# Performance work log

Hardware: AMD Instinct MI355X
Metric: run time of the kernel (lower is better)

The kernel has to match this reference:

```python
import jax, jax.numpy as jnp
import numpy as np

NUM_NODES = 116
EMBED = 64
HIDDEN = 64
OUT_FEAT = 116


def mish(x):
    return x * jnp.tanh(jax.nn.softplus(x))


def sage_conv(x, src, dst, w_l, b_l, w_r, n):
    # PyG SAGEConv (mean aggr): out = lin_l(mean_{j->i} x_j) + lin_r(x_i)
    agg = jax.ops.segment_sum(x[src], dst, num_segments=n)
    cnt = jax.ops.segment_sum(jnp.ones((src.shape[0],), x.dtype), dst, num_segments=n)
    mean = agg / jnp.clip(cnt, 1.0)[:, None]
    return mean @ w_l.T + b_l + x @ w_r.T


def setup_inputs() -> dict:
    key = jax.random.key(0)
    ks = jax.random.split(key, 12)
    B = 64
    N = B * NUM_NODES          # 7424 total nodes
    E = N * 32                 # 237568 edges
    d_in = EMBED * NUM_NODES   # 7424
    d_hid = HIDDEN * NUM_NODES # 7424
    d_out = OUT_FEAT * NUM_NODES  # 13456

    def lin_w(k, fan_out, fan_in):
        s = 1.0 / np.sqrt(fan_in)
        return jax.random.uniform(k, (fan_out, fan_in), jnp.float32, -s, s)

    return {
        "z": jax.random.normal(ks[0], (N, EMBED), jnp.float32),
        "edge_index": jax.random.randint(ks[1], (2, E), 0, N, jnp.int64),
        "batch_size": B,
        "w1_l": lin_w(ks[2], EMBED, EMBED),
        "b1_l": jnp.zeros((EMBED,), jnp.float32),
        "w1_r": lin_w(ks[3], EMBED, EMBED),
        "w2_l": lin_w(ks[4], EMBED, EMBED),
        "b2_l": jnp.zeros((EMBED,), jnp.float32),
        "w2_r": lin_w(ks[5], EMBED, EMBED),
        "fc1_w": lin_w(ks[6], d_hid, d_in),
        "fc1_b": jax.random.uniform(ks[7], (d_hid,), jnp.float32, -1/np.sqrt(d_in), 1/np.sqrt(d_in)),
        "fc2_w": lin_w(ks[8], d_out, d_hid),
        "fc2_b": jax.random.uniform(ks[9], (d_out,), jnp.float32, -1/np.sqrt(d_hid), 1/np.sqrt(d_hid)),
    }


def reference(z, edge_index, batch_size, w1_l, b1_l, w1_r, w2_l, b2_l, w2_r,
              fc1_w, fc1_b, fc2_w, fc2_b):
    n = z.shape[0]
    src, dst = edge_index[0], edge_index[1]
    h = mish(sage_conv(z, src, dst, w1_l, b1_l, w1_r, n))
    h = mish(sage_conv(h, src, dst, w2_l, b2_l, w2_r, n))
    h_flat = h.reshape(batch_size, NUM_NODES * EMBED)
    hidden = mish(h_flat @ fc1_w.T + fc1_b)
    x_rec = (hidden @ fc2_w.T + fc2_b).reshape(batch_size, NUM_NODES, OUT_FEAT)
    # enforce symmetry, unit diagonal
    sym = 0.5 * (x_rec + jnp.swapaxes(x_rec, 1, 2))
    eye = jnp.eye(NUM_NODES, dtype=bool)[None]
    sym = jnp.where(eye, jnp.asarray(1.0, sym.dtype), sym)
    return sym.reshape(batch_size * NUM_NODES, OUT_FEAT)
```

## Files before the change

### kernel.cpp

```cpp
#include <hip/hip_runtime.h>
#include <math.h>

#define NODES_TOT 7424
#define EDGES     237568
#define BATCH     64
#define NN        116
#define KDIM      7424
#define N1        7424
#define N2        13456
#define NKB       116
#define KSPLIT1   16
#define KSPLIT2   8

typedef __attribute__((ext_vector_type(8))) short bf16x8;
typedef __attribute__((ext_vector_type(4))) float f32x4;
typedef __attribute__((ext_vector_type(4))) short s16x4;

__device__ __forceinline__ float mish_f(float v) {
    float sp = fmaxf(v, 0.0f) + log1pf(expf(-fabsf(v)));
    return v * tanhf(sp);
}

__device__ __forceinline__ unsigned short bf_rne(float f) {
    unsigned u = __float_as_uint(f);
    u += 0x7fffu + ((u >> 16) & 1u);
    return (unsigned short)(u >> 16);
}

__global__ void zero_kernel(int* __restrict__ p, int n) {
    int i = blockIdx.x * 256 + threadIdx.x;
    if (i < n) p[i] = 0;
}

__global__ void hist_kernel(const int* __restrict__ dst, int* __restrict__ hist) {
    int e = blockIdx.x * 256 + threadIdx.x;
    if (e < EDGES) atomicAdd(&hist[dst[e]], 1);
}

__global__ void scan_kernel(const int* __restrict__ hist, int* __restrict__ row_start,
                            int* __restrict__ cursor) {
    __shared__ int s[1024];
    int t = threadIdx.x;
    int base = t * 8;
    int loc[8];
    int sum = 0;
    #pragma unroll
    for (int c = 0; c < 8; ++c) {
        int idx = base + c;
        int v = (idx < NODES_TOT) ? hist[idx] : 0;
        loc[c] = sum;
        sum += v;
    }
    s[t] = sum;
    __syncthreads();
    for (int off = 1; off < 1024; off <<= 1) {
        int v = (t >= off) ? s[t - off] : 0;
        __syncthreads();
        s[t] += v;
        __syncthreads();
    }
    int excl = s[t] - sum;
    #pragma unroll
    for (int c = 0; c < 8; ++c) {
        int idx = base + c;
        if (idx < NODES_TOT) {
            int r = excl + loc[c];
            row_start[idx] = r;
            cursor[idx] = r;
        }
    }
}

__global__ void csr_fill_kernel(const int* __restrict__ src, const int* __restrict__ dst,
                                int* __restrict__ cursor, int* __restrict__ csr_src) {
    int e = blockIdx.x * 256 + threadIdx.x;
    if (e < EDGES) {
        int p = atomicAdd(&cursor[dst[e]], 1);
        csr_src[p] = src[e];
    }
}

template <bool BF>
__global__ void __launch_bounds__(256) conv_kernel(
        const float* __restrict__ x, const int* __restrict__ csr_src,
        const int* __restrict__ row_start, const int* __restrict__ deg_arr,
        const float* __restrict__ w_l, const float* __restrict__ b_l,
        const float* __restrict__ w_r, void* __restrict__ h_out_v) {
    __shared__ float wlT[64 * 64];
    __shared__ float wrT[64 * 64];
    __shared__ float mv[4][64];
    __shared__ float xv[4][64];
    int t = threadIdx.x;
    for (int i = 0; i < 16; ++i) {
        int idx = t + i * 256;
        int f = idx >> 6, k = idx & 63;
        wlT[k * 64 + f] = w_l[idx];
        wrT[k * 64 + f] = w_r[idx];
    }
    int g = t >> 6, f = t & 63;
    __syncthreads();
    for (int nb = blockIdx.x * 4; nb < NODES_TOT; nb += gridDim.x * 4) {
        int node = nb + g;
        int deg = deg_arr[node];
        int rs = row_start[node];
        float sum = 0.f;
        for (int e = 0; e < deg; ++e) {
            int s = csr_src[rs + e];
            sum += x[s * 64 + f];
        }
        float mean = sum / (float)max(deg, 1);
        mv[g][f] = mean;
        xv[g][f] = x[node * 64 + f];
        __syncthreads();
        float o = b_l[f];
        #pragma unroll
        for (int k = 0; k < 64; ++k) {
            o = fmaf(mv[g][k], wlT[k * 64 + f], o);
            o = fmaf(xv[g][k], wrT[k * 64 + f], o);
        }
        float m = mish_f(o);
        if (BF) ((unsigned short*)h_out_v)[node * 64 + f] = bf_rne(m);
        else    ((float*)h_out_v)[node * 64 + f] = m;
        __syncthreads();
    }
}

template <int KSHIFT>
__global__ void __launch_bounds__(256) gemm_tile(
        const unsigned short* __restrict__ Abf, const float* __restrict__ W,
        float* __restrict__ Cp, int N) {
    __shared__ __align__(16) short Wsh[512 * 8];
    int t = threadIdx.x;
    int bx = blockIdx.x, by = blockIdx.y;
    int kb0 = (by * NKB) >> KSHIFT;
    int kb1 = ((by + 1) * NKB) >> KSHIFT;
    int n0 = bx * 64;
    int r = t >> 2, q = t & 3;
    int wr = n0 + r; if (wr >= N) wr = N - 1;
    const float* wsrc = W + (size_t)wr * KDIM + q * 4;
    int half = q & 1;
    int fbase = q >> 1;
    int wv = t >> 6, l = t & 63, l15 = l & 15, hi = l >> 4;
    f32x4 acc[4];
    #pragma unroll
    for (int g = 0; g < 4; ++g) acc[g] = (f32x4){0.f, 0.f, 0.f, 0.f};

    f32x4 w[4];
    {
        size_t k0 = (size_t)kb0 * 64;
        #pragma unroll
        for (int i = 0; i < 4; ++i) w[i] = *(const f32x4*)(wsrc + k0 + i * 16);
    }
    for (int kb = kb0; kb < kb1; ++kb) {
        s16x4 cv[4];
        #pragma unroll
        for (int i = 0; i < 4; ++i)
            #pragma unroll
            for (int j = 0; j < 4; ++j) cv[i][j] = (short)bf_rne(w[i][j]);
        __syncthreads();
        #pragma unroll
        for (int i = 0; i < 4; ++i)
            *(s16x4*)&Wsh[((i * 2 + fbase) * 64 + r) * 8 + half * 4] = cv[i];
        __syncthreads();
        if (kb + 1 < kb1) {
            size_t kn = (size_t)(kb + 1) * 64;
            #pragma unroll
            for (int i = 0; i < 4; ++i) w[i] = *(const f32x4*)(wsrc + kn + i * 16);
        }
        size_t k0 = (size_t)kb * 64;
        #pragma unroll
        for (int s = 0; s < 2; ++s) {
            int fw = s * 4 + hi;
            bf16x8 bh = *(const bf16x8*)&Wsh[(fw * 64 + wv * 16 + l15) * 8];
            #pragma unroll
            for (int g = 0; g < 4; ++g) {
                bf16x8 av = *(const bf16x8*)(Abf + (size_t)(g * 16 + l15) * KDIM + k0 + fw * 8);
                acc[g] = __builtin_amdgcn_mfma_f32_16x16x32_bf16(av, bh, acc[g], 0, 0, 0);
            }
        }
    }
    int gn = n0 + wv * 16 + l15;
    if (gn < N) {
        float* cp = Cp + (size_t)by * 64 * N;
        #pragma unroll
        for (int g = 0; g < 4; ++g)
            #pragma unroll
            for (int rr = 0; rr < 4; ++rr)
                cp[(size_t)(g * 16 + hi * 4 + rr) * N + gn] = acc[g][rr];
    }
}

__global__ void reduce1_kernel(const float* __restrict__ Cp, const float* __restrict__ b,
                               unsigned short* __restrict__ A2) {
    int i4 = (blockIdx.x * 256 + threadIdx.x) * 4;
    if (i4 >= BATCH * N1) return;
    int n = i4 % N1;
    f32x4 acc = *(const f32x4*)(b + n);
    #pragma unroll
    for (int s = 0; s < KSPLIT1; ++s)
        acc += *(const f32x4*)(Cp + (size_t)s * BATCH * N1 + i4);
    s16x4 o;
    #pragma unroll
    for (int j = 0; j < 4; ++j) o[j] = (short)bf_rne(mish_f(acc[j]));
    *(s16x4*)(A2 + i4) = o;
}

__global__ void reduce2_kernel(const float* __restrict__ Cp, const float* __restrict__ b,
                               float* __restrict__ C2) {
    int i4 = (blockIdx.x * 256 + threadIdx.x) * 4;
    if (i4 >= BATCH * N2) return;
    int n = i4 % N2;
    f32x4 acc = *(const f32x4*)(b + n);
    #pragma unroll
    for (int s = 0; s < KSPLIT2; ++s)
        acc += *(const f32x4*)(Cp + (size_t)s * BATCH * N2 + i4);
    *(f32x4*)(C2 + i4) = acc;
}

__global__ void sym_kernel(const float* __restrict__ C2, float* __restrict__ out) {
    int tid = blockIdx.x * 256 + threadIdx.x;
    if (tid >= BATCH * NN * NN) return;
    int j = tid % NN;
    int r = tid / NN;
    int i = r % NN;
    int b = r / NN;
    float v;
    if (i == j) {
        v = 1.0f;
    } else {
        v = 0.5f * (C2[(size_t)b * N2 + i * NN + j] + C2[(size_t)b * N2 + j * NN + i]);
    }
    out[tid] = v;
}

extern "C" void kernel_launch(void* const* d_in, const int* in_sizes, int n_in,
                              void* d_out, int out_size, void* d_ws, size_t ws_size,
                              hipStream_t stream) {
    const float* z     = (const float*)d_in[0];
    const int*   edge  = (const int*)d_in[1];
    const float* w1_l  = (const float*)d_in[3];
    const float* b1_l  = (const float*)d_in[4];
    const float* w1_r  = (const float*)d_in[5];
    const float* w2_l  = (const float*)d_in[6];
    const float* b2_l  = (const float*)d_in[7];
    const float* w2_r  = (const float*)d_in[8];
    const float* fc1_w = (const float*)d_in[9];
    const float* fc1_b = (const float*)d_in[10];
    const float* fc2_w = (const float*)d_in[11];
    const float* fc2_b = (const float*)d_in[12];
    float* out = (float*)d_out;

    char* ws = (char*)d_ws;
    size_t off = 0;
    auto alloc = [&](size_t bytes) {
        void* p = ws + off;
        off = (off + bytes + 255) & ~(size_t)255;
        return p;
    };
    int*            hist      = (int*)alloc(NODES_TOT * 4);
    int*            row_start = (int*)alloc(NODES_TOT * 4);
    int*            cursor    = (int*)alloc(NODES_TOT * 4);
    int*            csr_src   = (int*)alloc((size_t)EDGES * 4);
    float*          h1        = (float*)alloc((size_t)NODES_TOT * 64 * 4);
    unsigned short* A1        = (unsigned short*)alloc((size_t)NODES_TOT * 64 * 2);
    float*          Cp1       = (float*)alloc((size_t)KSPLIT1 * BATCH * N1 * 4);
    unsigned short* A2        = (unsigned short*)alloc((size_t)BATCH * N1 * 2);
    float*          Cp2       = (float*)alloc((size_t)KSPLIT2 * BATCH * N2 * 4);
    float*          C2        = (float*)alloc((size_t)BATCH * N2 * 4);

    const int* src = edge;
    const int* dst = edge + EDGES;

    zero_kernel<<<(NODES_TOT + 255) / 256, 256, 0, stream>>>(hist, NODES_TOT);
    hist_kernel<<<(EDGES + 255) / 256, 256, 0, stream>>>(dst, hist);
    scan_kernel<<<1, 1024, 0, stream>>>(hist, row_start, cursor);
    csr_fill_kernel<<<(EDGES + 255) / 256, 256, 0, stream>>>(src, dst, cursor, csr_src);

    conv_kernel<false><<<928, 256, 0, stream>>>(z, csr_src, row_start, hist, w1_l, b1_l, w1_r, h1);
    conv_kernel<true><<<928, 256, 0, stream>>>(h1, csr_src, row_start, hist, w2_l, b2_l, w2_r, A1);

    gemm_tile<4><<<dim3(N1 / 64, KSPLIT1), 256, 0, stream>>>(A1, fc1_w, Cp1, N1);
    reduce1_kernel<<<(BATCH * N1 / 4 + 255) / 256, 256, 0, stream>>>(Cp1, fc1_b, A2);

    gemm_tile<3><<<dim3((N2 + 63) / 64, KSPLIT2), 256, 0, stream>>>(A2, fc2_w, Cp2, N2);
    reduce2_kernel<<<(BATCH * N2 / 4 + 255) / 256, 256, 0, stream>>>(Cp2, fc2_b, C2);

    sym_kernel<<<(BATCH * NN * NN + 255) / 256, 256, 0, stream>>>(C2, out);
}
```

Measured before the change: 390.4 us.

## Double-buffer weight and activation tiles in LDS and reduce fc1 split-K

The fc GEMM kernel now stages both the fp32->bf16 converted weight tile and the bf16 activation tile in double-buffered LDS. Global loads for the next two K-steps are issued ahead of the MFMA phase, and the barrier is a custom lgkmcnt wait plus s_barrier. Activation reads previously went straight to global memory; they now come from shared memory. fc1's split-K drops from 16 to 8, which halves the partial-sum traffic and reduce work but gives the first GEMM fewer blocks to spread across the chip.

After: 324.4 us. 1.2x faster.

```diff
diff --git a/kernel.cpp b/kernel.cpp
--- a/kernel.cpp
+++ b/kernel.cpp
@@ -9,8 +9,7 @@
 #define N1        7424
 #define N2        13456
 #define NKB       116
-#define KSPLIT1   16
-#define KSPLIT2   8
+#define KSPLIT    8
 
 typedef __attribute__((ext_vector_type(8))) short bf16x8;
 typedef __attribute__((ext_vector_type(4))) float f32x4;
@@ -129,56 +128,99 @@
 __global__ void __launch_bounds__(256) gemm_tile(
         const unsigned short* __restrict__ Abf, const float* __restrict__ W,
         float* __restrict__ Cp, int N) {
-    __shared__ __align__(16) short Wsh[512 * 8];
+    __shared__ __align__(16) short Wsh[2][4096];
+    __shared__ __align__(16) short Ash[2][4096];
     int t = threadIdx.x;
     int bx = blockIdx.x, by = blockIdx.y;
     int kb0 = (by * NKB) >> KSHIFT;
     int kb1 = ((by + 1) * NKB) >> KSHIFT;
+    int S = kb1 - kb0;
     int n0 = bx * 64;
     int r = t >> 2, q = t & 3;
     int wr = n0 + r; if (wr >= N) wr = N - 1;
-    const float* wsrc = W + (size_t)wr * KDIM + q * 4;
-    int half = q & 1;
-    int fbase = q >> 1;
+    const float*          wsrc = W   + (size_t)wr * KDIM + (size_t)kb0 * 64 + q * 4;
+    const unsigned short* asrc = Abf + (size_t)r  * KDIM + (size_t)kb0 * 64 + q * 8;
+    int fb = q >> 1, hf = q & 1;
     int wv = t >> 6, l = t & 63, l15 = l & 15, hi = l >> 4;
     f32x4 acc[4];
     #pragma unroll
     for (int g = 0; g < 4; ++g) acc[g] = (f32x4){0.f, 0.f, 0.f, 0.f};
 
-    f32x4 w[4];
-    {
-        size_t k0 = (size_t)kb0 * 64;
-        #pragma unroll
-        for (int i = 0; i < 4; ++i) w[i] = *(const f32x4*)(wsrc + k0 + i * 16);
-    }
-    for (int kb = kb0; kb < kb1; ++kb) {
-        s16x4 cv[4];
-        #pragma unroll
-        for (int i = 0; i < 4; ++i)
-            #pragma unroll
-            for (int j = 0; j < 4; ++j) cv[i][j] = (short)bf_rne(w[i][j]);
-        __syncthreads();
-        #pragma unroll
-        for (int i = 0; i < 4; ++i)
-            *(s16x4*)&Wsh[((i * 2 + fbase) * 64 + r) * 8 + half * 4] = cv[i];
-        __syncthreads();
-        if (kb + 1 < kb1) {
-            size_t kn = (size_t)(kb + 1) * 64;
-            #pragma unroll
-            for (int i = 0; i < 4; ++i) w[i] = *(const f32x4*)(wsrc + kn + i * 16);
-        }
-        size_t k0 = (size_t)kb * 64;
-        #pragma unroll
-        for (int s = 0; s < 2; ++s) {
-            int fw = s * 4 + hi;
-            bf16x8 bh = *(const bf16x8*)&Wsh[(fw * 64 + wv * 16 + l15) * 8];
-            #pragma unroll
-            for (int g = 0; g < 4; ++g) {
-                bf16x8 av = *(const bf16x8*)(Abf + (size_t)(g * 16 + l15) * KDIM + k0 + fw * 8);
-                acc[g] = __builtin_amdgcn_mfma_f32_16x16x32_bf16(av, bh, acc[g], 0, 0, 0);
-            }
-        }
-    }
+    f32x4 wA0, wA1, wA2, wA3, wB0, wB1, wB2, wB3;
+    bf16x8 aA0, aA1, aB0, aB1;
+
+#define ISSUE(W0, W1, W2, W3, A0, A1, step) do {                          \
+        size_t kk = (size_t)(step) * 64;                                  \
+        W0 = *(const f32x4*)(wsrc + kk);                                  \
+        W1 = *(const f32x4*)(wsrc + kk + 16);                             \
+        W2 = *(const f32x4*)(wsrc + kk + 32);                             \
+        W3 = *(const f32x4*)(wsrc + kk + 48);                             \
+        A0 = *(const bf16x8*)(asrc + kk);                                 \
+        A1 = *(const bf16x8*)(asrc + kk + 32);                            \
+    } while (0)
+
+#define CONVWRITE(W0, W1, W2, W3, A0, A1, b) do {                         \
+        s16x4 cv0, cv1, cv2, cv3;                                         \
+        _Pragma("unroll")                                                 \
+        for (int j = 0; j < 4; ++j) {                                     \
+            cv0[j] = (short)bf_rne(W0[j]);                                \
+            cv1[j] = (short)bf_rne(W1[j]);                                \
+            cv2[j] = (short)bf_rne(W2[j]);                                \
+            cv3[j] = (short)bf_rne(W3[j]);                                \
+        }                                                                 \
+        *(s16x4*)&Wsh[b][((0 * 2 + fb) * 64 + r) * 8 + hf * 4] = cv0;     \
+        *(s16x4*)&Wsh[b][((1 * 2 + fb) * 64 + r) * 8 + hf * 4] = cv1;     \
+        *(s16x4*)&Wsh[b][((2 * 2 + fb) * 64 + r) * 8 + hf * 4] = cv2;     \
+        *(s16x4*)&Wsh[b][((3 * 2 + fb) * 64 + r) * 8 + hf * 4] = cv3;     \
+        *(bf16x8*)&Ash[b][(q * 64 + r) * 8] = A0;                         \
+        *(bf16x8*)&Ash[b][((q + 4) * 64 + r) * 8] = A1;                   \
+    } while (0)
+
+#define MFMAPH(b) do {                                                    \
+        _Pragma("unroll")                                                 \
+        for (int s = 0; s < 2; ++s) {                                     \
+            int fw = s * 4 + hi;                                          \
+            bf16x8 bh = *(const bf16x8*)&Wsh[b][(fw * 64 + wv * 16 + l15) * 8]; \
+            _Pragma("unroll")                                             \
+            for (int g = 0; g < 4; ++g) {                                 \
+                bf16x8 av = *(const bf16x8*)&Ash[b][(fw * 64 + g * 16 + l15) * 8]; \
+                acc[g] = __builtin_amdgcn_mfma_f32_16x16x32_bf16(av, bh, acc[g], 0, 0, 0); \
+            }                                                             \
+        }                                                                 \
+    } while (0)
+
+#define BAR() asm volatile("s_waitcnt lgkmcnt(0)\n\ts_barrier" ::: "memory")
+
+    ISSUE(wA0, wA1, wA2, wA3, aA0, aA1, 0);
+    ISSUE(wB0, wB1, wB2, wB3, aB0, aB1, 1);
+    CONVWRITE(wA0, wA1, wA2, wA3, aA0, aA1, 0);
+    BAR();
+
+    int i = 0;
+    for (; i + 1 < S - 1; i += 2) {
+        if (i + 2 < S) ISSUE(wA0, wA1, wA2, wA3, aA0, aA1, i + 2);
+        MFMAPH(0);
+        CONVWRITE(wB0, wB1, wB2, wB3, aB0, aB1, 1);
+        BAR();
+        if (i + 3 < S) ISSUE(wB0, wB1, wB2, wB3, aB0, aB1, i + 3);
+        MFMAPH(1);
+        CONVWRITE(wA0, wA1, wA2, wA3, aA0, aA1, 0);
+        BAR();
+    }
+    if (i < S - 1) {
+        MFMAPH(0);
+        CONVWRITE(wB0, wB1, wB2, wB3, aB0, aB1, 1);
+        BAR();
+        MFMAPH(1);
+    } else {
+        MFMAPH(0);
+    }
+
+#undef ISSUE
+#undef CONVWRITE
+#undef MFMAPH
+#undef BAR
+
     int gn = n0 + wv * 16 + l15;
     if (gn < N) {
         float* cp = Cp + (size_t)by * 64 * N;
@@ -197,7 +239,7 @@
     int n = i4 % N1;
     f32x4 acc = *(const f32x4*)(b + n);
     #pragma unroll
-    for (int s = 0; s < KSPLIT1; ++s)
+    for (int s = 0; s < KSPLIT; ++s)
         acc += *(const f32x4*)(Cp + (size_t)s * BATCH * N1 + i4);
     s16x4 o;
     #pragma unroll
@@ -212,7 +254,7 @@
     int n = i4 % N2;
     f32x4 acc = *(const f32x4*)(b + n);
     #pragma unroll
-    for (int s = 0; s < KSPLIT2; ++s)
+    for (int s = 0; s < KSPLIT; ++s)
         acc += *(const f32x4*)(Cp + (size_t)s * BATCH * N2 + i4);
     *(f32x4*)(C2 + i4) = acc;
 }
@@ -263,9 +305,9 @@
     int*            csr_src   = (int*)alloc((size_t)EDGES * 4);
     float*          h1        = (float*)alloc((size_t)NODES_TOT * 64 * 4);
     unsigned short* A1        = (unsigned short*)alloc((size_t)NODES_TOT * 64 * 2);
-    float*          Cp1       = (float*)alloc((size_t)KSPLIT1 * BATCH * N1 * 4);
+    float*          Cp1       = (float*)alloc((size_t)KSPLIT * BATCH * N1 * 4);
     unsigned short* A2        = (unsigned short*)alloc((size_t)BATCH * N1 * 2);
-    float*          Cp2       = (float*)alloc((size_t)KSPLIT2 * BATCH * N2 * 4);
+    float*          Cp2       = (float*)alloc((size_t)KSPLIT * BATCH * N2 * 4);
     float*          C2        = (float*)alloc((size_t)BATCH * N2 * 4);
 
     const int* src = edge;
@@ -279,10 +321,10 @@
     conv_kernel<false><<<928, 256, 0, stream>>>(z, csr_src, row_start, hist, w1_l, b1_l, w1_r, h1);
     conv_kernel<true><<<928, 256, 0, stream>>>(h1, csr_src, row_start, hist, w2_l, b2_l, w2_r, A1);
 
-    gemm_tile<4><<<dim3(N1 / 64, KSPLIT1), 256, 0, stream>>>(A1, fc1_w, Cp1, N1);
+    gemm_tile<3><<<dim3(N1 / 64, KSPLIT), 256, 0, stream>>>(A1, fc1_w, Cp1, N1);
     reduce1_kernel<<<(BATCH * N1 / 4 + 255) / 256, 256, 0, stream>>>(Cp1, fc1_b, A2);
 
-    gemm_tile<3><<<dim3((N2 + 63) / 64, KSPLIT2), 256, 0, stream>>>(A2, fc2_w, Cp2, N2);
+    gemm_tile<3><<<dim3((N2 + 63) / 64, KSPLIT), 256, 0, stream>>>(A2, fc2_w, Cp2, N2);
     reduce2_kernel<<<(BATCH * N2 / 4 + 255) / 256, 256, 0, stream>>>(Cp2, fc2_b, C2);
 
     sym_kernel<<<(BATCH * NN * NN + 255) / 256, 256, 0, stream>>>(C2, out);
```

## Stream GEMM operand tiles via global_load_lds double buffering and halve K-split

Applied to the files above, without the earlier changes.

Replaces the register-staged weight tile loader with direct global-to-LDS DMA loads (global_load_lds) for both the fp32 weight tile and the bf16 activation tile. The loads are double-buffered, with XOR swizzles to avoid bank conflicts and a vmcnt-based wait scheme. Weights are now converted to bf16 after being read from LDS instead of before the LDS store. The K-split factors are halved, which gives fewer partial-sum buffers to reduce but also fewer blocks to fill the device.

Measured after the change: 333.5 us. -14.6%, faster.

```diff
diff --git a/kernel.cpp b/kernel.cpp
--- a/kernel.cpp
+++ b/kernel.cpp
@@ -9,8 +9,8 @@
 #define N1        7424
 #define N2        13456
 #define NKB       116
-#define KSPLIT1   16
-#define KSPLIT2   8
+#define KSPLIT1   8
+#define KSPLIT2   4
 
 typedef __attribute__((ext_vector_type(8))) short bf16x8;
 typedef __attribute__((ext_vector_type(4))) float f32x4;
@@ -25,6 +25,12 @@
     unsigned u = __float_as_uint(f);
     u += 0x7fffu + ((u >> 16) & 1u);
     return (unsigned short)(u >> 16);
+}
+
+__device__ __forceinline__ void gload_lds16(const void* g, void* l) {
+    __builtin_amdgcn_global_load_lds(
+        (const __attribute__((address_space(1))) void*)g,
+        (__attribute__((address_space(3))) void*)l, 16, 0, 0);
 }
 
 __global__ void zero_kernel(int* __restrict__ p, int n) {
@@ -125,60 +131,104 @@
     }
 }
 
-template <int KSHIFT>
-__global__ void __launch_bounds__(256) gemm_tile(
+template <int KS>
+__global__ void __launch_bounds__(256) gemm_dma(
         const unsigned short* __restrict__ Abf, const float* __restrict__ W,
         float* __restrict__ Cp, int N) {
-    __shared__ __align__(16) short Wsh[512 * 8];
+    __shared__ __align__(16) float          Wlds[2][4096];
+    __shared__ __align__(16) unsigned short Alds[2][4096];
     int t = threadIdx.x;
     int bx = blockIdx.x, by = blockIdx.y;
-    int kb0 = (by * NKB) >> KSHIFT;
-    int kb1 = ((by + 1) * NKB) >> KSHIFT;
+    int kb0 = (by * NKB) / KS;
+    int kb1 = ((by + 1) * NKB) / KS;
+    int S = kb1 - kb0;
     int n0 = bx * 64;
-    int r = t >> 2, q = t & 3;
-    int wr = n0 + r; if (wr >= N) wr = N - 1;
-    const float* wsrc = W + (size_t)wr * KDIM + q * 4;
-    int half = q & 1;
-    int fbase = q >> 1;
     int wv = t >> 6, l = t & 63, l15 = l & 15, hi = l >> 4;
+
+    const float* wsrc[4];
+    #pragma unroll
+    for (int ii = 0; ii < 4; ++ii) {
+        int rloc = wv * 16 + ii * 4 + (l >> 4);
+        int wr = n0 + rloc; if (wr >= N) wr = N - 1;
+        int g = (l & 15) ^ ((rloc & 7) << 1);
+        wsrc[ii] = W + (size_t)wr * KDIM + (size_t)kb0 * 64 + g * 4;
+    }
+    const unsigned short* asrcp[2];
+    #pragma unroll
+    for (int ii = 0; ii < 2; ++ii) {
+        int rloc = wv * 16 + ii * 8 + (l >> 3);
+        int g = (l & 7) ^ (rloc & 7);
+        asrcp[ii] = Abf + (size_t)rloc * KDIM + (size_t)kb0 * 64 + g * 8;
+    }
+
     f32x4 acc[4];
     #pragma unroll
     for (int g = 0; g < 4; ++g) acc[g] = (f32x4){0.f, 0.f, 0.f, 0.f};
 
-    f32x4 w[4];
-    {
-        size_t k0 = (size_t)kb0 * 64;
-        #pragma unroll
-        for (int i = 0; i < 4; ++i) w[i] = *(const f32x4*)(wsrc + k0 + i * 16);
-    }
-    for (int kb = kb0; kb < kb1; ++kb) {
-        s16x4 cv[4];
-        #pragma unroll
-        for (int i = 0; i < 4; ++i)
-            #pragma unroll
-            for (int j = 0; j < 4; ++j) cv[i][j] = (short)bf_rne(w[i][j]);
-        __syncthreads();
-        #pragma unroll
-        for (int i = 0; i < 4; ++i)
-            *(s16x4*)&Wsh[((i * 2 + fbase) * 64 + r) * 8 + half * 4] = cv[i];
-        __syncthreads();
-        if (kb + 1 < kb1) {
-            size_t kn = (size_t)(kb + 1) * 64;
-            #pragma unroll
-            for (int i = 0; i < 4; ++i) w[i] = *(const f32x4*)(wsrc + kn + i * 16);
-        }
-        size_t k0 = (size_t)kb * 64;
-        #pragma unroll
-        for (int s = 0; s < 2; ++s) {
-            int fw = s * 4 + hi;
-            bf16x8 bh = *(const bf16x8*)&Wsh[(fw * 64 + wv * 16 + l15) * 8];
-            #pragma unroll
-            for (int g = 0; g < 4; ++g) {
-                bf16x8 av = *(const bf16x8*)(Abf + (size_t)(g * 16 + l15) * KDIM + k0 + fw * 8);
-                acc[g] = __builtin_amdgcn_mfma_f32_16x16x32_bf16(av, bh, acc[g], 0, 0, 0);
-            }
-        }
-    }
+#define ISSUE(step, buf) do {                                              \
+        size_t ko = (size_t)(step) * 64;                                   \
+        _Pragma("unroll")                                                  \
+        for (int ii = 0; ii < 4; ++ii)                                     \
+            gload_lds16(wsrc[ii] + ko, &Wlds[buf][(wv * 16 + ii * 4) * 64]); \
+        _Pragma("unroll")                                                  \
+        for (int ii = 0; ii < 2; ++ii)                                     \
+            gload_lds16(asrcp[ii] + ko, &Alds[buf][(wv * 16 + ii * 8) * 64]); \
+    } while (0)
+
+#define MFMAPH(buf) do {                                                   \
+        _Pragma("unroll")                                                  \
+        for (int s = 0; s < 2; ++s) {                                      \
+            int fw = s * 4 + hi;                                           \
+            int n = wv * 16 + l15;                                         \
+            int g0 = (2 * fw) ^ ((n & 7) << 1);                            \
+            f32x4 wlo = *(const f32x4*)&Wlds[buf][n * 64 + g0 * 4];        \
+            f32x4 whi = *(const f32x4*)&Wlds[buf][n * 64 + g0 * 4 + 4];    \
+            bf16x8 bh;                                                     \
+            _Pragma("unroll")                                              \
+            for (int j = 0; j < 4; ++j) {                                  \
+                bh[j]     = (short)bf_rne(wlo[j]);                         \
+                bh[4 + j] = (short)bf_rne(whi[j]);                         \
+            }                                                              \
+            _Pragma("unroll")                                              \
+            for (int g = 0; g < 4; ++g) {                                  \
+                int ar = g * 16 + l15;                                     \
+                bf16x8 av = *(const bf16x8*)&Alds[buf][ar * 64 + ((fw ^ (ar & 7)) * 8)]; \
+                acc[g] = __builtin_amdgcn_mfma_f32_16x16x32_bf16(av, bh, acc[g], 0, 0, 0); \
+            }                                                              \
+        }                                                                  \
+    } while (0)
+
+#define WAIT6()  asm volatile("s_waitcnt vmcnt(6)" ::: "memory")
+#define WAIT0()  asm volatile("s_waitcnt vmcnt(0)" ::: "memory")
+#define RBAR()   asm volatile("s_barrier" ::: "memory")
+#define LBAR()   asm volatile("s_waitcnt lgkmcnt(0)\n\ts_barrier" ::: "memory")
+
+    ISSUE(0, 0);
+    ISSUE(1, 1);
+    WAIT6();
+    RBAR();
+
+    int i = 0;
+    while (true) {
+        MFMAPH(0);
+        LBAR();
+        if (i + 2 < S) { ISSUE(i + 2, 0); WAIT6(); } else { WAIT0(); }
+        RBAR();
+        if (++i == S) break;
+        MFMAPH(1);
+        LBAR();
+        if (i + 2 < S) { ISSUE(i + 2, 1); WAIT6(); } else { WAIT0(); }
+        RBAR();
+        if (++i == S) break;
+    }
+
+#undef ISSUE
+#undef MFMAPH
+#undef WAIT6
+#undef WAIT0
+#undef RBAR
+#undef LBAR
+
     int gn = n0 + wv * 16 + l15;
     if (gn < N) {
         float* cp = Cp + (size_t)by * 64 * N;
@@ -279,10 +329,10 @@
     conv_kernel<false><<<928, 256, 0, stream>>>(z, csr_src, row_start, hist, w1_l, b1_l, w1_r, h1);
     conv_kernel<true><<<928, 256, 0, stream>>>(h1, csr_src, row_start, hist, w2_l, b2_l, w2_r, A1);
 
-    gemm_tile<4><<<dim3(N1 / 64, KSPLIT1), 256, 0, stream>>>(A1, fc1_w, Cp1, N1);
+    gemm_dma<KSPLIT1><<<dim3(N1 / 64, KSPLIT1), 256, 0, stream>>>(A1, fc1_w, Cp1, N1);
     reduce1_kernel<<<(BATCH * N1 / 4 + 255) / 256, 256, 0, stream>>>(Cp1, fc1_b, A2);
 
-    gemm_tile<3><<<dim3((N2 + 63) / 64, KSPLIT2), 256, 0, stream>>>(A2, fc2_w, Cp2, N2);
+    gemm_dma<KSPLIT2><<<dim3((N2 + 63) / 64, KSPLIT2), 256, 0, stream>>>(A2, fc2_w, Cp2, N2);
     reduce2_kernel<<<(BATCH * N2 / 4 + 255) / 256, 256, 0, stream>>>(Cp2, fc2_b, C2);
 
     sym_kernel<<<(BATCH * NN * NN + 255) / 256, 256, 0, stream>>>(C2, out);
```

## Double-buffer larger K chunks in weight GEMM with fewer split-K partitions

Applied to the files above, without the earlier changes.

Replaces the per-64-element K step GEMM with a kernel that stages 256-wide K super-blocks of the fp32 weights, converted to bf16, into a double-buffered LDS array. The next chunk's global loads overlap the current chunk's MFMAs, and activation loads are software-pipelined. Split-K factors drop from 16/8 to 4/2, which shrinks the partial-sum buffers the reduce kernels must read. The cost is fewer blocks in the grid (less parallelism to hide latency), higher register pressure from 16 f32x4 prefetch registers, and a hand-written waitcnt/barrier.

Result: slower. 423.5 us (+8.5%).

```diff
diff --git a/kernel.cpp b/kernel.cpp
--- a/kernel.cpp
+++ b/kernel.cpp
@@ -8,9 +8,9 @@
 #define KDIM      7424
 #define N1        7424
 #define N2        13456
-#define NKB       116
-#define KSPLIT1   16
-#define KSPLIT2   8
+#define SUPER     29
+#define KSPLIT1   4
+#define KSPLIT2   2
 
 typedef __attribute__((ext_vector_type(8))) short bf16x8;
 typedef __attribute__((ext_vector_type(4))) float f32x4;
@@ -125,60 +125,93 @@
     }
 }
 
-template <int KSHIFT>
-__global__ void __launch_bounds__(256) gemm_tile(
+template <int KS>
+__global__ void __launch_bounds__(256, 2) gemm_big(
         const unsigned short* __restrict__ Abf, const float* __restrict__ W,
         float* __restrict__ Cp, int N) {
-    __shared__ __align__(16) short Wsh[512 * 8];
+    __shared__ __align__(16) unsigned short Wlds[2][16384];
     int t = threadIdx.x;
     int bx = blockIdx.x, by = blockIdx.y;
-    int kb0 = (by * NKB) >> KSHIFT;
-    int kb1 = ((by + 1) * NKB) >> KSHIFT;
+    int sb0 = (by * SUPER) / KS;
+    int sb1 = ((by + 1) * SUPER) / KS;
+    int S = sb1 - sb0;
     int n0 = bx * 64;
     int r = t >> 2, q = t & 3;
     int wr = n0 + r; if (wr >= N) wr = N - 1;
-    const float* wsrc = W + (size_t)wr * KDIM + q * 4;
-    int half = q & 1;
-    int fbase = q >> 1;
+    const float* wsrc = W + (size_t)wr * KDIM + (size_t)sb0 * 256 + q * 4;
     int wv = t >> 6, l = t & 63, l15 = l & 15, hi = l >> 4;
+    const unsigned short* arow[4];
+    #pragma unroll
+    for (int g = 0; g < 4; ++g)
+        arow[g] = Abf + (size_t)(g * 16 + l15) * KDIM + (size_t)sb0 * 256 + hi * 8;
+
     f32x4 acc[4];
     #pragma unroll
     for (int g = 0; g < 4; ++g) acc[g] = (f32x4){0.f, 0.f, 0.f, 0.f};
 
-    f32x4 w[4];
-    {
-        size_t k0 = (size_t)kb0 * 64;
-        #pragma unroll
-        for (int i = 0; i < 4; ++i) w[i] = *(const f32x4*)(wsrc + k0 + i * 16);
-    }
-    for (int kb = kb0; kb < kb1; ++kb) {
-        s16x4 cv[4];
-        #pragma unroll
-        for (int i = 0; i < 4; ++i)
-            #pragma unroll
-            for (int j = 0; j < 4; ++j) cv[i][j] = (short)bf_rne(w[i][j]);
-        __syncthreads();
-        #pragma unroll
-        for (int i = 0; i < 4; ++i)
-            *(s16x4*)&Wsh[((i * 2 + fbase) * 64 + r) * 8 + half * 4] = cv[i];
-        __syncthreads();
-        if (kb + 1 < kb1) {
-            size_t kn = (size_t)(kb + 1) * 64;
-            #pragma unroll
-            for (int i = 0; i < 4; ++i) w[i] = *(const f32x4*)(wsrc + kn + i * 16);
+    f32x4 w[16];
+
+#define LOADW(s) do {                                                      \
+        size_t ko = (size_t)(s) * 256;                                     \
+        _Pragma("unroll")                                                  \
+        for (int j = 0; j < 16; ++j)                                       \
+            w[j] = *(const f32x4*)(wsrc + ko + j * 16);                    \
+    } while (0)
+
+#define CONVW(nb) do {                                                     \
+        _Pragma("unroll")                                                  \
+        for (int j = 0; j < 16; ++j) {                                     \
+            s16x4 cv;                                                      \
+            _Pragma("unroll")                                              \
+            for (int e = 0; e < 4; ++e) cv[e] = (short)bf_rne(w[j][e]);    \
+            *(s16x4*)&Wlds[nb][((2 * j + (q >> 1)) * 64 + r) * 8 + (q & 1) * 4] = cv; \
+        }                                                                  \
+    } while (0)
+
+#define MFMA_STEP(b, s) do {                                               \
+        size_t ko = (size_t)(s) * 256;                                     \
+        bf16x8 a0 = *(const bf16x8*)(arow[0] + ko);                        \
+        bf16x8 a1 = *(const bf16x8*)(arow[1] + ko);                        \
+        bf16x8 a2 = *(const bf16x8*)(arow[2] + ko);                        \
+        bf16x8 a3 = *(const bf16x8*)(arow[3] + ko);                        \
+        _Pragma("unroll")                                                  \
+        for (int kk = 0; kk < 8; ++kk) {                                   \
+            bf16x8 n0_, n1_, n2_, n3_;                                     \
+            if (kk < 7) {                                                  \
+                n0_ = *(const bf16x8*)(arow[0] + ko + (kk + 1) * 32);      \
+                n1_ = *(const bf16x8*)(arow[1] + ko + (kk + 1) * 32);      \
+                n2_ = *(const bf16x8*)(arow[2] + ko + (kk + 1) * 32);      \
+                n3_ = *(const bf16x8*)(arow[3] + ko + (kk + 1) * 32);      \
+            }                                                              \
+            bf16x8 bh = *(const bf16x8*)&Wlds[b][((kk * 4 + hi) * 64 + wv * 16 + l15) * 8]; \
+            acc[0] = __builtin_amdgcn_mfma_f32_16x16x32_bf16(a0, bh, acc[0], 0, 0, 0); \
+            acc[1] = __builtin_amdgcn_mfma_f32_16x16x32_bf16(a1, bh, acc[1], 0, 0, 0); \
+            acc[2] = __builtin_amdgcn_mfma_f32_16x16x32_bf16(a2, bh, acc[2], 0, 0, 0); \
+            acc[3] = __builtin_amdgcn_mfma_f32_16x16x32_bf16(a3, bh, acc[3], 0, 0, 0); \
+            if (kk < 7) { a0 = n0_; a1 = n1_; a2 = n2_; a3 = n3_; }        \
+        }                                                                  \
+    } while (0)
+
+#define LBAR() asm volatile("s_waitcnt lgkmcnt(0)\n\ts_barrier" ::: "memory")
+
+    LOADW(0);
+    CONVW(0);
+    LBAR();
+    for (int s = 0; s < S; ++s) {
+        int b = s & 1;
+        if (s + 1 < S) LOADW(s + 1);
+        MFMA_STEP(b, s);
+        if (s + 1 < S) {
+            CONVW(b ^ 1);
+            LBAR();
         }
-        size_t k0 = (size_t)kb * 64;
-        #pragma unroll
-        for (int s = 0; s < 2; ++s) {
-            int fw = s * 4 + hi;
-            bf16x8 bh = *(const bf16x8*)&Wsh[(fw * 64 + wv * 16 + l15) * 8];
-            #pragma unroll
-            for (int g = 0; g < 4; ++g) {
-                bf16x8 av = *(const bf16x8*)(Abf + (size_t)(g * 16 + l15) * KDIM + k0 + fw * 8);
-                acc[g] = __builtin_amdgcn_mfma_f32_16x16x32_bf16(av, bh, acc[g], 0, 0, 0);
-            }
-        }
-    }
+    }
+
+#undef LOADW
+#undef CONVW
+#undef MFMA_STEP
+#undef LBAR
+
     int gn = n0 + wv * 16 + l15;
     if (gn < N) {
         float* cp = Cp + (size_t)by * 64 * N;
@@ -279,10 +312,10 @@
     conv_kernel<false><<<928, 256, 0, stream>>>(z, csr_src, row_start, hist, w1_l, b1_l, w1_r, h1);
     conv_kernel<true><<<928, 256, 0, stream>>>(h1, csr_src, row_start, hist, w2_l, b2_l, w2_r, A1);
 
-    gemm_tile<4><<<dim3(N1 / 64, KSPLIT1), 256, 0, stream>>>(A1, fc1_w, Cp1, N1);
+    gemm_big<KSPLIT1><<<dim3(N1 / 64, KSPLIT1), 256, 0, stream>>>(A1, fc1_w, Cp1, N1);
     reduce1_kernel<<<(BATCH * N1 / 4 + 255) / 256, 256, 0, stream>>>(Cp1, fc1_b, A2);
 
-    gemm_tile<3><<<dim3((N2 + 63) / 64, KSPLIT2), 256, 0, stream>>>(A2, fc2_w, Cp2, N2);
+    gemm_big<KSPLIT2><<<dim3((N2 + 63) / 64, KSPLIT2), 256, 0, stream>>>(A2, fc2_w, Cp2, N2);
     reduce2_kernel<<<(BATCH * N2 / 4 + 255) / 256, 256, 0, stream>>>(Cp2, fc2_b, C2);
 
     sym_kernel<<<(BATCH * NN * NN + 255) / 256, 256, 0, stream>>>(C2, out);
```
